# Performance work log

Measured on AMD Instinct MI355X. Metric: run time of the kernel, lower is better.

The kernel has to match this reference:

```python
import jax, jax.numpy as jnp
from jax import lax
import numpy as np

DEPTH, D_MODEL, D_INNER, D_STATE, DT_RANK = 24, 192, 384, 16, 12
EPS = 1e-5

def _layernorm(x, w, b):
    m = x.mean(-1, keepdims=True)
    v = ((x - m) ** 2).mean(-1, keepdims=True)
    return (x - m) * lax.rsqrt(v + EPS) * w + b

def _silu(x):
    return x * jax.nn.sigmoid(x)

def _mamba_mixer(x, in_w, cw, cb, xp_w, dtw, dtb, a_log, dvec, out_w):
    # x: (B, L, D_MODEL)
    B, L, _ = x.shape
    xz = jnp.einsum('bld,ed->ble', x, in_w)            # (B, L, 2*D_INNER)
    xi, z = xz[..., :D_INNER], xz[..., D_INNER:]
    # causal depthwise conv1d, kernel 4 (left-pad 3, truncate to L)
    xt = jnp.moveaxis(xi, 1, 2)                        # (B, D_INNER, L)
    xt = jnp.pad(xt, ((0, 0), (0, 0), (3, 0)))
    xt = lax.conv_general_dilated(xt, cw[:, None, :], (1,), 'VALID',
                                  dimension_numbers=('NCH', 'OIH', 'NCH'),
                                  feature_group_count=D_INNER)
    xt = _silu(xt + cb[None, :, None])
    xc = jnp.moveaxis(xt, 1, 2)                        # (B, L, D_INNER)
    x_dbl = jnp.einsum('bld,ed->ble', xc, xp_w)        # (B, L, DT_RANK+2*D_STATE)
    dt = x_dbl[..., :DT_RANK]
    Bm = x_dbl[..., DT_RANK:DT_RANK + D_STATE]         # (B, L, N)
    Cm = x_dbl[..., DT_RANK + D_STATE:]                # (B, L, N)
    delta = jax.nn.softplus(jnp.einsum('blr,dr->bld', dt, dtw) + dtb)  # (B, L, D_INNER)
    A = -jnp.exp(a_log)                                # (D_INNER, N)
    dA = jnp.exp(delta[..., None] * A)                 # (B, L, D_INNER, N)
    dBx = (delta * xc)[..., None] * Bm[:, :, None, :]  # (B, L, D_INNER, N)

    def step(h, inp):
        dA_t, dBx_t, C_t = inp
        h = dA_t * h + dBx_t
        y = jnp.einsum('bdn,bn->bd', h, C_t)
        return h, y

    h0 = jnp.zeros((B, D_INNER, D_STATE), x.dtype)
    _, ys = lax.scan(step, h0, (jnp.moveaxis(dA, 1, 0), jnp.moveaxis(dBx, 1, 0), jnp.moveaxis(Cm, 1, 0)))
    y = jnp.moveaxis(ys, 0, 1) + xc * dvec             # (B, L, D_INNER)
    y = y * _silu(z)
    return jnp.einsum('ble,de->bld', y, out_w)

def _forward(x, patch_w, patch_b, norm_w, norm_b, in_proj_w, conv_w, conv_b,
             x_proj_w, dt_w, dt_b, A_log, Dp, out_proj_w, normf_w, normf_b, head_w, head_b):
    # patch embed: conv 16x16 stride 16 -> (B, 192, 14, 14) -> (B, 196, 192)
    h = lax.conv_general_dilated(x, patch_w, (16, 16), 'VALID',
                                 dimension_numbers=('NCHW', 'OIHW', 'NCHW'))
    h = h + patch_b[None, :, None, None]
    B = h.shape[0]
    hidden = h.reshape(B, D_MODEL, -1).transpose(0, 2, 1)  # (B, L, D)
    residual = None
    for d in range(DEPTH):
        residual = hidden if residual is None else residual + hidden
        normed = _layernorm(residual, norm_w[d], norm_b[d])
        hidden = _mamba_mixer(normed, in_proj_w[d], conv_w[d], conv_b[d], x_proj_w[d],
                              dt_w[d], dt_b[d], A_log[d], Dp[d], out_proj_w[d])
    residual = residual + hidden
    feat = _layernorm(residual, normf_w, normf_b)
    pooled = feat.mean(axis=1)                           # final_pool_type='mean'
    return pooled @ head_w.T + head_b                    # (B, num_classes)

def setup_inputs() -> dict:
    key = jax.random.key(0)
    ks = jax.random.split(key, 16)
    s = 0.05
    return {
        'x': jax.random.normal(ks[0], (64, 3, 224, 224), jnp.float32),
        'patch_w': jax.random.normal(ks[1], (192, 3, 16, 16), jnp.float32) * s,
        'patch_b': jnp.zeros((192,), jnp.float32),
        'norm_w': jnp.ones((DEPTH, D_MODEL), jnp.float32),
        'norm_b': jnp.zeros((DEPTH, D_MODEL), jnp.float32),
        'in_proj_w': jax.random.normal(ks[2], (DEPTH, 2 * D_INNER, D_MODEL), jnp.float32) * s,
        'conv_w': jax.random.normal(ks[3], (DEPTH, D_INNER, 4), jnp.float32) * 0.3,
        'conv_b': jnp.zeros((DEPTH, D_INNER), jnp.float32),
        'x_proj_w': jax.random.normal(ks[4], (DEPTH, DT_RANK + 2 * D_STATE, D_INNER), jnp.float32) * s,
        'dt_w': jax.random.normal(ks[5], (DEPTH, D_INNER, DT_RANK), jnp.float32) * s,
        'dt_b': jax.random.uniform(ks[6], (DEPTH, D_INNER), jnp.float32, -4.0, -2.0),
        'A_log': jnp.log(jnp.broadcast_to(jnp.arange(1, D_STATE + 1, dtype=jnp.float32), (DEPTH, D_INNER, D_STATE))),
        'Dp': jnp.ones((DEPTH, D_INNER), jnp.float32),
        'out_proj_w': jax.random.normal(ks[7], (DEPTH, D_MODEL, D_INNER), jnp.float32) * s,
        'normf_w': jnp.ones((D_MODEL,), jnp.float32),
        'normf_b': jnp.zeros((D_MODEL,), jnp.float32),
        'head_w': jax.random.normal(ks[8], (1000, D_MODEL), jnp.float32) * s,
        'head_b': jnp.zeros((1000,), jnp.float32),
    }

def reference(x, patch_w, patch_b, norm_w, norm_b, in_proj_w, conv_w, conv_b,
              x_proj_w, dt_w, dt_b, A_log, Dp, out_proj_w, normf_w, normf_b, head_w, head_b):
    return _forward(x, patch_w, patch_b, norm_w, norm_b, in_proj_w, conv_w, conv_b,
                    x_proj_w, dt_w, dt_b, A_log, Dp, out_proj_w, normf_w, normf_b, head_w, head_b)
```

## Files before the change

### kernel.cpp

```cpp
#include <hip/hip_runtime.h>
#include <math.h>


#define DEPTH 24
#define DM 192
#define DI 384
#define DS 16
#define DR 12
#define SEQL 196
#define BATCH 64
#define MROWS (BATCH*SEQL)
#define XDP 8624
#define LOG2E 1.44269504088896340736f

typedef unsigned short ushort_t;
typedef __bf16 bf16x8 __attribute__((ext_vector_type(8)));
typedef float f32x4 __attribute__((ext_vector_type(4)));

__device__ __forceinline__ float sigmoidf_(float x) { return 1.f / (1.f + __expf(-x)); }

__device__ __forceinline__ ushort_t f2bf(float f) {
    union { float f; unsigned u; } c; c.f = f;
    unsigned u = c.u;
    return (ushort_t)((u + 0x7FFFu + ((u >> 16) & 1u)) >> 16);
}
__device__ __forceinline__ float bf2f(ushort_t u) {
    union { unsigned u; float f; } c; c.u = ((unsigned)u) << 16;
    return c.f;
}

__device__ __forceinline__ void load_lds16(const ushort_t* g, ushort_t* l) {
    __builtin_amdgcn_global_load_lds((__attribute__((address_space(1))) void*)g,
                                     (__attribute__((address_space(3))) void*)l, 16, 0, 0);
}

template<int CTRL>
__device__ __forceinline__ float dpp_mov(float oldv, float src) {
    return __builtin_bit_cast(float, __builtin_amdgcn_update_dpp(
        __builtin_bit_cast(int, oldv), __builtin_bit_cast(int, src),
        CTRL, 0xF, 0xF, false));
}

template<int CTRL, bool LAST>
__device__ __forceinline__ void ks_step(float* P, float* h) {
    #pragma unroll
    for (int n = 0; n < DS; n++) {
        float Hp = dpp_mov<CTRL>(0.f, h[n]);
        float Pp = LAST ? 1.f : dpp_mov<CTRL>(1.f, P[n]);
        h[n] = fmaf(P[n], Hp, h[n]);
        if (!LAST) P[n] *= Pp;
    }
}

__global__ void f2bf4_kernel(const float* __restrict__ src, ushort_t* __restrict__ dst, int n4) {
    int i = blockIdx.x * 256 + threadIdx.x;
    if (i >= n4) return;
    float4 v = ((const float4*)src)[i];
    union { ushort_t s[4]; uint2 u; } o;
    o.s[0] = f2bf(v.x); o.s[1] = f2bf(v.y); o.s[2] = f2bf(v.z); o.s[3] = f2bf(v.w);
    ((uint2*)dst)[i] = o.u;
}

__global__ void xp_pad_kernel(const float* __restrict__ src, ushort_t* __restrict__ dst) {
    int i = blockIdx.x * 256 + threadIdx.x;
    if (i >= DEPTH * 64 * 384) return;
    int col = i % 384, row = (i / 384) & 63, d = i / (384 * 64);
    float v = (row < 44) ? src[(size_t)d * 44 * 384 + row * 384 + col] : 0.f;
    dst[i] = f2bf(v);
}

template<bool BF>
__global__ void ln_kernel(float* __restrict__ residual, const float* __restrict__ hidden,
                          const float* __restrict__ w, const float* __restrict__ b,
                          void* __restrict__ out_) {
    int wave = threadIdx.x >> 6, lane = threadIdx.x & 63;
    int row = blockIdx.x * 4 + wave;
    float* rr = residual + (size_t)row * DM;
    const float* hr = hidden + (size_t)row * DM;
    float v0 = rr[lane]       + hr[lane];
    float v1 = rr[lane + 64]  + hr[lane + 64];
    float v2 = rr[lane + 128] + hr[lane + 128];
    rr[lane] = v0; rr[lane + 64] = v1; rr[lane + 128] = v2;
    float s = v0 + v1 + v2;
    #pragma unroll
    for (int off = 32; off > 0; off >>= 1) s += __shfl_down(s, off);
    float mean = __shfl(s, 0) * (1.f / DM);
    float d0 = v0 - mean, d1 = v1 - mean, d2 = v2 - mean;
    float q = d0 * d0 + d1 * d1 + d2 * d2;
    #pragma unroll
    for (int off = 32; off > 0; off >>= 1) q += __shfl_down(q, off);
    float rstd = rsqrtf(__shfl(q, 0) * (1.f / DM) + 1e-5f);
    float o0 = d0 * rstd * w[lane]       + b[lane];
    float o1 = d1 * rstd * w[lane + 64]  + b[lane + 64];
    float o2 = d2 * rstd * w[lane + 128] + b[lane + 128];
    if constexpr (BF) {
        ushort_t* o = (ushort_t*)out_ + (size_t)row * DM;
        o[lane] = f2bf(o0); o[lane + 64] = f2bf(o1); o[lane + 128] = f2bf(o2);
    } else {
        float* o = (float*)out_ + (size_t)row * DM;
        o[lane] = o0; o[lane + 64] = o1; o[lane + 128] = o2;
    }
}

template<int BN, int WM, int WN, int NST, bool TC>
__global__ __launch_bounds__(256, 2) void gemm_mfma(const ushort_t* __restrict__ A,
        const ushort_t* __restrict__ W, float* __restrict__ C, int K, int ldC) {
    constexpr int FM = 128 / (WM * 16);
    constexpr int FN = BN / (WN * 16);
    __shared__ ushort_t sA[128 * 32];
    __shared__ ushort_t sB[BN * 32];
    const int t = threadIdx.x;
    const int wave = t >> 6, lane = t & 63;
    const int lr = lane & 15, lq = lane >> 4;
    const int wr = wave / WN, wc = wave % WN;
    const int m0 = blockIdx.x * 128, n0 = blockIdx.y * BN;
    const int wbase = t & ~63;

    f32x4 acc[FM][FN];
    #pragma unroll
    for (int i = 0; i < FM; i++)
        #pragma unroll
        for (int j = 0; j < FN; j++) acc[i][j] = f32x4{0.f, 0.f, 0.f, 0.f};

    for (int k0 = 0; k0 < K; k0 += 32) {
        __syncthreads();
        #pragma unroll
        for (int c = 0; c < 2; c++) {
            int s = c * 256 + t;
            int row = s >> 2;
            int quad = (s & 3) ^ ((row >> 1) & 3);
            load_lds16(A + (size_t)(m0 + row) * K + k0 + quad * 8,
                       sA + (size_t)(c * 256 + wbase) * 8);
        }
        #pragma unroll
        for (int c = 0; c < BN * 4 / 256; c++) {
            int s = c * 256 + t;
            int row = s >> 2;
            int quad = (s & 3) ^ ((row >> 1) & 3);
            load_lds16(W + (size_t)(n0 + row) * K + k0 + quad * 8,
                       sB + (size_t)(c * 256 + wbase) * 8);
        }
        __syncthreads();
        bf16x8 af[FM], bfr[FN];
        #pragma unroll
        for (int i = 0; i < FM; i++) {
            int row = wr * FM * 16 + i * 16 + lr;
            int slot = (row << 2) | (lq ^ ((row >> 1) & 3));
            af[i] = *(const bf16x8*)&sA[(size_t)slot * 8];
        }
        #pragma unroll
        for (int j = 0; j < FN; j++) {
            int row = wc * FN * 16 + j * 16 + lr;
            int slot = (row << 2) | (lq ^ ((row >> 1) & 3));
            bfr[j] = *(const bf16x8*)&sB[(size_t)slot * 8];
        }
        #pragma unroll
        for (int i = 0; i < FM; i++)
            #pragma unroll
            for (int j = 0; j < FN; j++)
                acc[i][j] = __builtin_amdgcn_mfma_f32_16x16x32_bf16(af[i], bfr[j], acc[i][j], 0, 0, 0);
    }
    int crow0 = m0 + wr * FM * 16 + lq * 4;
    int ccol0 = n0 + wc * FN * 16 + lr;
    if constexpr (TC) {
        #pragma unroll
        for (int i = 0; i < FM; i++) {
            int m = crow0 + i * 16;
            int bb = m / 196, l = m % 196;
            #pragma unroll
            for (int j = 0; j < FN; j++) {
                int col = ccol0 + j * 16;
                if (col < 44) {
                    float4 v = {acc[i][j][0], acc[i][j][1], acc[i][j][2], acc[i][j][3]};
                    *(float4*)(C + (size_t)bb * XDP + (size_t)col * 196 + l) = v;
                }
            }
        }
    } else {
        #pragma unroll
        for (int i = 0; i < FM; i++)
            #pragma unroll
            for (int j = 0; j < FN; j++) {
                if (wc * FN + j >= NST) continue;
                float* cp = C + (size_t)(crow0 + i * 16) * ldC + ccol0 + j * 16;
                #pragma unroll
                for (int r = 0; r < 4; r++) cp[(size_t)r * ldC] = acc[i][j][r];
            }
    }
}

__global__ __launch_bounds__(256, 2) void gemm_patch_mfma(const ushort_t* __restrict__ Xbf,
        const ushort_t* __restrict__ Wbf, const float* __restrict__ bias, float* __restrict__ C) {
    constexpr int FM = 2, FN = 4;
    __shared__ ushort_t sA[128 * 32];
    __shared__ ushort_t sB[64 * 32];
    const int t = threadIdx.x;
    const int wave = t >> 6, lane = t & 63;
    const int lr = lane & 15, lq = lane >> 4;
    const int m0 = blockIdx.x * 128, n0 = blockIdx.y * 64;
    const int wbase = t & ~63;

    const ushort_t* abase[2];
    int aquad[2];
    #pragma unroll
    for (int c = 0; c < 2; c++) {
        int s = c * 256 + t;
        int row = s >> 2;
        aquad[c] = (s & 3) ^ ((row >> 1) & 3);
        int m = m0 + row;
        int b = m / 196, r = m % 196, py = r / 14, px = r % 14;
        abase[c] = Xbf + (size_t)b * 150528 + py * 3584 + px * 16;
    }
    int brow = t >> 2;
    int bquad = (t & 3) ^ ((brow >> 1) & 3);
    const ushort_t* bbase = Wbf + (size_t)(n0 + brow) * 768 + bquad * 8;

    f32x4 acc[FM][FN];
    #pragma unroll
    for (int i = 0; i < FM; i++)
        #pragma unroll
        for (int j = 0; j < FN; j++) acc[i][j] = f32x4{0.f, 0.f, 0.f, 0.f};

    for (int k0 = 0; k0 < 768; k0 += 32) {
        __syncthreads();
        #pragma unroll
        for (int c = 0; c < 2; c++) {
            int k = k0 + aquad[c] * 8;
            int ci = k >> 8, ky = (k >> 4) & 15, kx0 = k & 15;
            load_lds16(abase[c] + ci * 50176 + ky * 224 + kx0,
                       sA + (size_t)(c * 256 + wbase) * 8);
        }
        load_lds16(bbase + k0, sB + (size_t)wbase * 8);
        __syncthreads();
        bf16x8 af[FM], bfr[FN];
        #pragma unroll
        for (int i = 0; i < FM; i++) {
            int row = wave * FM * 16 + i * 16 + lr;
            int slot = (row << 2) | (lq ^ ((row >> 1) & 3));
            af[i] = *(const bf16x8*)&sA[(size_t)slot * 8];
        }
        #pragma unroll
        for (int j = 0; j < FN; j++) {
            int row = j * 16 + lr;
            int slot = (row << 2) | (lq ^ ((row >> 1) & 3));
            bfr[j] = *(const bf16x8*)&sB[(size_t)slot * 8];
        }
        #pragma unroll
        for (int i = 0; i < FM; i++)
            #pragma unroll
            for (int j = 0; j < FN; j++)
                acc[i][j] = __builtin_amdgcn_mfma_f32_16x16x32_bf16(af[i], bfr[j], acc[i][j], 0, 0, 0);
    }
    int crow0 = m0 + wave * FM * 16 + lq * 4;
    int ccol0 = n0 + lr;
    #pragma unroll
    for (int i = 0; i < FM; i++)
        #pragma unroll
        for (int j = 0; j < FN; j++) {
            int col = ccol0 + j * 16;
            float bv = bias[col];
            float* cp = C + (size_t)(crow0 + i * 16) * DM + col;
            #pragma unroll
            for (int r = 0; r < 4; r++) cp[(size_t)r * DM] = acc[i][j][r] + bv;
        }
}

template<bool BIAS>
__global__ __launch_bounds__(256, 2) void gemm64(const float* __restrict__ A,
        const float* __restrict__ W, const float* __restrict__ bias,
        float* __restrict__ C, int M, int N, int K) {
    __shared__ float As[32][68];
    __shared__ float Ws[32][68];
    int t = threadIdx.x;
    int m0 = blockIdx.x * 64, n0 = blockIdx.y * 64;
    int lr = t >> 2, lk = (t & 3) * 4;
    int am = m0 + lr; bool avld = am < M;
    const float* Ap = A + (size_t)(avld ? am : 0) * K + lk;
    int wn = n0 + lr; bool wv = wn < N;
    const float* Wp = W + (size_t)(wv ? wn : 0) * K + lk;
    int tm = (t >> 4) * 4, tn = (t & 15) * 4;
    float acc[4][4];
    #pragma unroll
    for (int i = 0; i < 4; i++)
        #pragma unroll
        for (int j = 0; j < 4; j++) acc[i][j] = 0.f;

    for (int k0 = 0; k0 < K; k0 += 32) {
        float4 a0 = make_float4(0.f, 0.f, 0.f, 0.f), a1 = a0, w0 = a0, w1 = a0;
        if (avld) { a0 = *(const float4*)(Ap + k0); a1 = *(const float4*)(Ap + k0 + 16); }
        if (wv)   { w0 = *(const float4*)(Wp + k0); w1 = *(const float4*)(Wp + k0 + 16); }
        __syncthreads();
        As[lk + 0][lr] = a0.x; As[lk + 1][lr] = a0.y; As[lk + 2][lr] = a0.z; As[lk + 3][lr] = a0.w;
        As[lk + 16][lr] = a1.x; As[lk + 17][lr] = a1.y; As[lk + 18][lr] = a1.z; As[lk + 19][lr] = a1.w;
        Ws[lk + 0][lr] = w0.x; Ws[lk + 1][lr] = w0.y; Ws[lk + 2][lr] = w0.z; Ws[lk + 3][lr] = w0.w;
        Ws[lk + 16][lr] = w1.x; Ws[lk + 17][lr] = w1.y; Ws[lk + 18][lr] = w1.z; Ws[lk + 19][lr] = w1.w;
        __syncthreads();
        #pragma unroll
        for (int kk = 0; kk < 32; kk++) {
            float4 x0 = *(const float4*)&As[kk][tm];
            float4 y0 = *(const float4*)&Ws[kk][tn];
            float av[4] = {x0.x, x0.y, x0.z, x0.w};
            float bv[4] = {y0.x, y0.y, y0.z, y0.w};
            #pragma unroll
            for (int i = 0; i < 4; i++)
                #pragma unroll
                for (int j = 0; j < 4; j++) acc[i][j] = fmaf(av[i], bv[j], acc[i][j]);
        }
    }
    #pragma unroll
    for (int i = 0; i < 4; i++) {
        int m = m0 + tm + i;
        if (m >= M) continue;
        float* cr = C + (size_t)m * N;
        int n = n0 + tn;
        if (n < N) {
            float4 v = {acc[i][0], acc[i][1], acc[i][2], acc[i][3]};
            if (BIAS) { v.x += bias[n]; v.y += bias[n + 1]; v.z += bias[n + 2]; v.w += bias[n + 3]; }
            *(float4*)(cr + n) = v;
        }
    }
}

__global__ void conv_silu_kernel(const float* __restrict__ xz, const float* __restrict__ cw,
                                 const float* __restrict__ cb, ushort_t* __restrict__ xcbf) {
    int idx = blockIdx.x * 256 + threadIdx.x;
    if (idx >= MROWS * DI) return;
    int e = idx % DI; int bl = idx / DI; int l = bl % SEQL; int b = bl / SEQL;
    const float* base = xz + (size_t)(b * SEQL) * 768 + e;
    float w0 = cw[e * 4], w1 = cw[e * 4 + 1], w2 = cw[e * 4 + 2], w3 = cw[e * 4 + 3];
    float acc = cb[e];
    if (l >= 3) acc = fmaf(base[(size_t)(l - 3) * 768], w0, acc);
    if (l >= 2) acc = fmaf(base[(size_t)(l - 2) * 768], w1, acc);
    if (l >= 1) acc = fmaf(base[(size_t)(l - 1) * 768], w2, acc);
    acc = fmaf(base[(size_t)l * 768], w3, acc);
    xcbf[idx] = f2bf(acc * sigmoidf_(acc));
}

__global__ __launch_bounds__(512, 4) void scan_kernel(const float* __restrict__ xdt,
        const ushort_t* __restrict__ xcbf, const float* __restrict__ xz,
        const float* __restrict__ dtw, const float* __restrict__ dtb,
        const float* __restrict__ a_log, const float* __restrict__ Dp, ushort_t* __restrict__ y) {
    __shared__ float sd[44 * 196];
    __shared__ ushort_t zs[8 * 200];
    __shared__ ushort_t xcs[8 * 200];
    __shared__ ushort_t ys[8 * 200];
    __shared__ float avs[8][16];
    __shared__ float wdts[8][16];
    const int b = blockIdx.x, eg = blockIdx.y;
    const int tid = threadIdx.x;
    const int wave = tid >> 6, lane = tid & 63;
    const int e = eg * 8 + wave;

    {
        const float4* src4 = (const float4*)(xdt + (size_t)b * XDP);
        float4* sd4 = (float4*)sd;
        for (int i = tid; i < XDP / 4; i += 512) sd4[i] = src4[i];
    }
    if (lane < DS) avs[wave][lane] = -__expf(a_log[(size_t)e * DS + lane]) * LOG2E;
    if (lane >= 16 && lane < 16 + DR) wdts[wave][lane - 16] = dtw[(size_t)e * DR + (lane - 16)];
    if (tid < 196) {
        int l = tid;
        const ushort_t* xp = xcbf + (size_t)(b * SEQL + l) * DI + eg * 8;
        ushort4 xq0 = *(const ushort4*)xp;
        ushort4 xq1 = *(const ushort4*)(xp + 4);
        const float* zp = xz + (size_t)(b * SEQL + l) * 768 + DI + eg * 8;
        float4 zq0 = *(const float4*)zp;
        float4 zq1 = *(const float4*)(zp + 4);
        xcs[0 * 200 + l] = xq0.x; xcs[1 * 200 + l] = xq0.y;
        xcs[2 * 200 + l] = xq0.z; xcs[3 * 200 + l] = xq0.w;
        xcs[4 * 200 + l] = xq1.x; xcs[5 * 200 + l] = xq1.y;
        xcs[6 * 200 + l] = xq1.z; xcs[7 * 200 + l] = xq1.w;
        zs[0 * 200 + l] = f2bf(zq0.x); zs[1 * 200 + l] = f2bf(zq0.y);
        zs[2 * 200 + l] = f2bf(zq0.z); zs[3 * 200 + l] = f2bf(zq0.w);
        zs[4 * 200 + l] = f2bf(zq1.x); zs[5 * 200 + l] = f2bf(zq1.y);
        zs[6 * 200 + l] = f2bf(zq1.z); zs[7 * 200 + l] = f2bf(zq1.w);
    }
    __syncthreads();

    const float db = dtb[e];
    const bool act = lane < 49;
    const int lbase = act ? lane * 4 : 0;

    f32x4 dt4 = {db, db, db, db};
    #pragma unroll
    for (int k = 0; k < DR; k++) {
        f32x4 r = *(const f32x4*)&sd[k * 196 + lbase];
        dt4 += r * wdts[wave][k];
    }
    f32x4 d4;
    #pragma unroll
    for (int s = 0; s < 4; s++) {
        float v = dt4[s];
        d4[s] = (v > 20.f) ? v : __logf(1.f + __expf(v));
    }
    f32x4 du4;
    {
        ushort4 xcq = *(const ushort4*)&xcs[wave * 200 + lbase];
        du4 = d4 * f32x4{bf2f(xcq.x), bf2f(xcq.y), bf2f(xcq.z), bf2f(xcq.w)};
    }

    float P[DS], h[DS];
    #pragma unroll
    for (int n = 0; n < DS; n++) { P[n] = 1.f; h[n] = 0.f; }
    if (act) {
        #pragma unroll
        for (int n = 0; n < DS; n++) {
            float Avn = avs[wave][n];
            f32x4 Bn = *(const f32x4*)&sd[(12 + n) * 196 + lbase];
            float hn = 0.f, Pn = 1.f;
            #pragma unroll
            for (int s = 0; s < 4; s++) {
                float dA = __builtin_amdgcn_exp2f(d4[s] * Avn);
                hn = fmaf(hn, dA, du4[s] * Bn[s]);
                Pn *= dA;
            }
            P[n] = Pn; h[n] = hn;
        }
    }

    ks_step<0x111, false>(P, h);
    ks_step<0x112, false>(P, h);
    ks_step<0x114, false>(P, h);
    ks_step<0x118, false>(P, h);
    ks_step<0x142, false>(P, h);
    ks_step<0x143, true >(P, h);

    #pragma unroll
    for (int n = 0; n < DS; n++) {
        float Hp = __shfl_up(h[n], 1);
        h[n] = (lane == 0) ? 0.f : Hp;
    }

    if (act) {
        f32x4 acc4 = {0.f, 0.f, 0.f, 0.f};
        #pragma unroll
        for (int n = 0; n < DS; n++) {
            float Avn = avs[wave][n];
            f32x4 Bn = *(const f32x4*)&sd[(12 + n) * 196 + lbase];
            f32x4 Cn = *(const f32x4*)&sd[(28 + n) * 196 + lbase];
            float hn = h[n];
            #pragma unroll
            for (int s = 0; s < 4; s++) {
                float dA = __builtin_amdgcn_exp2f(d4[s] * Avn);
                hn = fmaf(hn, dA, du4[s] * Bn[s]);
                acc4[s] = fmaf(hn, Cn[s], acc4[s]);
            }
        }
        ushort4 xcq = *(const ushort4*)&xcs[wave * 200 + lbase];
        f32x4 xcv4 = {bf2f(xcq.x), bf2f(xcq.y), bf2f(xcq.z), bf2f(xcq.w)};
        ushort4 zq = *(const ushort4*)&zs[wave * 200 + lbase];
        f32x4 zv4 = {bf2f(zq.x), bf2f(zq.y), bf2f(zq.z), bf2f(zq.w)};
        const float Dv = Dp[e];
        ushort_t* yw = &ys[wave * 200 + lbase];
        #pragma unroll
        for (int s = 0; s < 4; s++) {
            float yv = fmaf(xcv4[s], Dv, acc4[s]);
            float zv = zv4[s];
            yw[s] = f2bf(yv * zv * sigmoidf_(zv));
        }
    }
    __syncthreads();
    if (tid < 196) {
        int l = tid;
        ushort4 o0, o1;
        o0.x = ys[0 * 200 + l]; o0.y = ys[1 * 200 + l];
        o0.z = ys[2 * 200 + l]; o0.w = ys[3 * 200 + l];
        o1.x = ys[4 * 200 + l]; o1.y = ys[5 * 200 + l];
        o1.z = ys[6 * 200 + l]; o1.w = ys[7 * 200 + l];
        ushort_t* yp = y + (size_t)(b * SEQL + l) * DI + eg * 8;
        *(ushort4*)yp = o0;
        *(ushort4*)(yp + 4) = o1;
    }
}

__global__ void pool_kernel(const float* __restrict__ normed, float* __restrict__ pooled) {
    int b = blockIdx.x, d = threadIdx.x;
    float s = 0.f;
    for (int l = 0; l < SEQL; l++) s += normed[(size_t)(b * SEQL + l) * DM + d];
    pooled[b * DM + d] = s * (1.f / 196.f);
}

extern "C" void kernel_launch(void* const* d_in, const int* in_sizes, int n_in,
                              void* d_out, int out_size, void* d_ws, size_t ws_size,
                              hipStream_t stream) {
    const float* x       = (const float*)d_in[0];
    const float* patch_w = (const float*)d_in[1];
    const float* patch_b = (const float*)d_in[2];
    const float* norm_w  = (const float*)d_in[3];
    const float* norm_b  = (const float*)d_in[4];
    const float* in_w    = (const float*)d_in[5];
    const float* conv_w  = (const float*)d_in[6];
    const float* conv_b  = (const float*)d_in[7];
    const float* xp_w    = (const float*)d_in[8];
    const float* dt_w    = (const float*)d_in[9];
    const float* dt_b    = (const float*)d_in[10];
    const float* A_log   = (const float*)d_in[11];
    const float* Dp      = (const float*)d_in[12];
    const float* out_w   = (const float*)d_in[13];
    const float* normf_w = (const float*)d_in[14];
    const float* normf_b = (const float*)d_in[15];
    const float* head_w  = (const float*)d_in[16];
    const float* head_b  = (const float*)d_in[17];

    float* ws = (float*)d_ws;
    float* residual     = ws;
    float* hidden       = ws + 2408448;
    float* xz           = ws + 4816896;
    ushort_t* xcbf      = (ushort_t*)(ws + 14450688);
    ushort_t* y_bf      = (ushort_t*)(ws + 16859136);
    ushort_t* x_bf      = (ushort_t*)(ws + 14450688);
    ushort_t* normed_bf = (ushort_t*)(ws + 19267584);
    float* xdbl_t       = ws + 20471808;
    float* pooled       = ws + 21023744;
    ushort_t* in_w_bf   = (ushort_t*)(ws + 21036032);
    ushort_t* out_w_bf  = (ushort_t*)(ws + 22805504);
    ushort_t* xp_w_bf   = (ushort_t*)(ws + 23690240);
    ushort_t* patch_w_bf= (ushort_t*)(ws + 23985152);

    (void)hipMemsetAsync(residual, 0, (size_t)2408448 * sizeof(float), stream);

    f2bf4_kernel<<<3456, 256, 0, stream>>>(in_w, in_w_bf, 884736);
    f2bf4_kernel<<<1728, 256, 0, stream>>>(out_w, out_w_bf, 442368);
    f2bf4_kernel<<<144, 256, 0, stream>>>(patch_w, patch_w_bf, 36864);
    f2bf4_kernel<<<9408, 256, 0, stream>>>(x, x_bf, 2408448);
    xp_pad_kernel<<<2304, 256, 0, stream>>>(xp_w, xp_w_bf);

    gemm_patch_mfma<<<dim3(98, 3), 256, 0, stream>>>(x_bf, patch_w_bf, patch_b, hidden);

    for (int d = 0; d < DEPTH; ++d) {
        ln_kernel<true><<<3136, 256, 0, stream>>>(residual, hidden, norm_w + d * DM,
                                                  norm_b + d * DM, normed_bf);
        gemm_mfma<192, 2, 2, 12, false><<<dim3(98, 4), 256, 0, stream>>>(normed_bf,
                in_w_bf + (size_t)d * 768 * 192, xz, 192, 768);
        conv_silu_kernel<<<18816, 256, 0, stream>>>(xz, conv_w + d * DI * 4, conv_b + d * DI, xcbf);
        gemm_mfma<64, 4, 1, 3, true><<<dim3(98, 1), 256, 0, stream>>>(xcbf,
                xp_w_bf + (size_t)d * 64 * 384, xdbl_t, 384, 196);
        scan_kernel<<<dim3(64, 48), 512, 0, stream>>>(xdbl_t, xcbf, xz, dt_w + d * DI * DR,
                dt_b + d * DI, A_log + d * DI * DS, Dp + d * DI, y_bf);
        gemm_mfma<64, 4, 1, 4, false><<<dim3(98, 3), 256, 0, stream>>>(y_bf,
                out_w_bf + (size_t)d * 192 * 384, hidden, 384, 192);
    }

    ln_kernel<false><<<3136, 256, 0, stream>>>(residual, hidden, normf_w, normf_b, xz);
    pool_kernel<<<64, 192, 0, stream>>>(xz, pooled);
    gemm64<true><<<dim3(1, 16), 256, 0, stream>>>(pooled, head_w, head_b, (float*)d_out, 64, 1000, 192);
}
```

Measured before the change: 3.167 ms.

## Remap selective scan lanes to state-by-time-chunk with DPP state reduction

```diff
diff --git a/kernel.cpp b/kernel.cpp
--- a/kernel.cpp
+++ b/kernel.cpp
@@ -41,15 +41,12 @@
         CTRL, 0xF, 0xF, false));
 }
 
-template<int CTRL, bool LAST>
-__device__ __forceinline__ void ks_step(float* P, float* h) {
-    #pragma unroll
-    for (int n = 0; n < DS; n++) {
-        float Hp = dpp_mov<CTRL>(0.f, h[n]);
-        float Pp = LAST ? 1.f : dpp_mov<CTRL>(1.f, P[n]);
-        h[n] = fmaf(P[n], Hp, h[n]);
-        if (!LAST) P[n] *= Pp;
-    }
+__device__ __forceinline__ float row16_sum(float v) {
+    v += dpp_mov<0xB1>(0.f, v);
+    v += dpp_mov<0x4E>(0.f, v);
+    v += dpp_mov<0x141>(0.f, v);
+    v += dpp_mov<0x140>(0.f, v);
+    return v;
 }
 
 __global__ void f2bf4_kernel(const float* __restrict__ src, ushort_t* __restrict__ dst, int n4) {
@@ -336,27 +333,27 @@
     xcbf[idx] = f2bf(acc * sigmoidf_(acc));
 }
 
-__global__ __launch_bounds__(512, 4) void scan_kernel(const float* __restrict__ xdt,
+__global__ __launch_bounds__(512, 6) void scan_kernel(const float* __restrict__ xdt,
         const ushort_t* __restrict__ xcbf, const float* __restrict__ xz,
         const float* __restrict__ dtw, const float* __restrict__ dtb,
         const float* __restrict__ a_log, const float* __restrict__ Dp, ushort_t* __restrict__ y) {
     __shared__ float sd[44 * 196];
+    __shared__ float dls[8][196];
     __shared__ ushort_t zs[8 * 200];
     __shared__ ushort_t xcs[8 * 200];
     __shared__ ushort_t ys[8 * 200];
-    __shared__ float avs[8][16];
     __shared__ float wdts[8][16];
     const int b = blockIdx.x, eg = blockIdx.y;
     const int tid = threadIdx.x;
     const int wave = tid >> 6, lane = tid & 63;
     const int e = eg * 8 + wave;
+    const int n = lane & 15, c = lane >> 4;
 
     {
         const float4* src4 = (const float4*)(xdt + (size_t)b * XDP);
         float4* sd4 = (float4*)sd;
         for (int i = tid; i < XDP / 4; i += 512) sd4[i] = src4[i];
     }
-    if (lane < DS) avs[wave][lane] = -__expf(a_log[(size_t)e * DS + lane]) * LOG2E;
     if (lane >= 16 && lane < 16 + DR) wdts[wave][lane - 16] = dtw[(size_t)e * DR + (lane - 16)];
     if (tid < 196) {
         int l = tid;
@@ -377,86 +374,85 @@
     }
     __syncthreads();
 
+    const float Avn = -__expf(a_log[(size_t)e * DS + n]) * LOG2E;
     const float db = dtb[e];
-    const bool act = lane < 49;
-    const int lbase = act ? lane * 4 : 0;
-
-    f32x4 dt4 = {db, db, db, db};
-    #pragma unroll
-    for (int k = 0; k < DR; k++) {
-        f32x4 r = *(const f32x4*)&sd[k * 196 + lbase];
-        dt4 += r * wdts[wave][k];
-    }
-    f32x4 d4;
-    #pragma unroll
-    for (int s = 0; s < 4; s++) {
-        float v = dt4[s];
-        d4[s] = (v > 20.f) ? v : __logf(1.f + __expf(v));
-    }
-    f32x4 du4;
+
+    if (lane < 49) {
+        const int lb = lane * 4;
+        f32x4 dt4 = {db, db, db, db};
+        #pragma unroll
+        for (int k = 0; k < DR; k++) {
+            f32x4 r = *(const f32x4*)&sd[k * 196 + lb];
+            dt4 += r * wdts[wave][k];
+        }
+        f32x4 d4;
+        #pragma unroll
+        for (int s = 0; s < 4; s++) {
+            float v = dt4[s];
+            d4[s] = (v > 20.f) ? v : __logf(1.f + __expf(v));
+        }
+        *(f32x4*)&dls[wave][lb] = d4;
+    }
+
+    const int t0 = (c == 0) ? 0 : 48 * c + 4;
+    const int iters = (c == 0) ? 13 : 12;
+    const float* Brow = &sd[(12 + n) * 196];
+    const float* Crow = &sd[(28 + n) * 196];
+    const float* dlw = dls[wave];
+    const ushort_t* xcw = &xcs[wave * 200];
+
+    float h = 0.f;
+    f32x4 dsum = {0.f, 0.f, 0.f, 0.f};
+    for (int i = 0; i < iters; i++) {
+        int t = t0 + 4 * i;
+        f32x4 dl = *(const f32x4*)&dlw[t];
+        f32x4 Bn = *(const f32x4*)&Brow[t];
+        ushort4 xcq = *(const ushort4*)&xcw[t];
+        const ushort_t* xcp = (const ushort_t*)&xcq;
+        dsum += dl;
+        #pragma unroll
+        for (int s = 0; s < 4; s++) {
+            float dA = __builtin_amdgcn_exp2f(dl[s] * Avn);
+            h = fmaf(h, dA, (dl[s] * bf2f(xcp[s])) * Bn[s]);
+        }
+    }
+    float P = __builtin_amdgcn_exp2f(Avn * (dsum[0] + dsum[1] + dsum[2] + dsum[3]));
+
     {
-        ushort4 xcq = *(const ushort4*)&xcs[wave * 200 + lbase];
-        du4 = d4 * f32x4{bf2f(xcq.x), bf2f(xcq.y), bf2f(xcq.z), bf2f(xcq.w)};
-    }
-
-    float P[DS], h[DS];
-    #pragma unroll
-    for (int n = 0; n < DS; n++) { P[n] = 1.f; h[n] = 0.f; }
-    if (act) {
-        #pragma unroll
-        for (int n = 0; n < DS; n++) {
-            float Avn = avs[wave][n];
-            f32x4 Bn = *(const f32x4*)&sd[(12 + n) * 196 + lbase];
-            float hn = 0.f, Pn = 1.f;
-            #pragma unroll
-            for (int s = 0; s < 4; s++) {
-                float dA = __builtin_amdgcn_exp2f(d4[s] * Avn);
-                hn = fmaf(hn, dA, du4[s] * Bn[s]);
-                Pn *= dA;
-            }
-            P[n] = Pn; h[n] = hn;
-        }
-    }
-
-    ks_step<0x111, false>(P, h);
-    ks_step<0x112, false>(P, h);
-    ks_step<0x114, false>(P, h);
-    ks_step<0x118, false>(P, h);
-    ks_step<0x142, false>(P, h);
-    ks_step<0x143, true >(P, h);
-
-    #pragma unroll
-    for (int n = 0; n < DS; n++) {
-        float Hp = __shfl_up(h[n], 1);
-        h[n] = (lane == 0) ? 0.f : Hp;
-    }
-
-    if (act) {
-        f32x4 acc4 = {0.f, 0.f, 0.f, 0.f};
-        #pragma unroll
-        for (int n = 0; n < DS; n++) {
-            float Avn = avs[wave][n];
-            f32x4 Bn = *(const f32x4*)&sd[(12 + n) * 196 + lbase];
-            f32x4 Cn = *(const f32x4*)&sd[(28 + n) * 196 + lbase];
-            float hn = h[n];
-            #pragma unroll
-            for (int s = 0; s < 4; s++) {
-                float dA = __builtin_amdgcn_exp2f(d4[s] * Avn);
-                hn = fmaf(hn, dA, du4[s] * Bn[s]);
-                acc4[s] = fmaf(hn, Cn[s], acc4[s]);
-            }
-        }
-        ushort4 xcq = *(const ushort4*)&xcs[wave * 200 + lbase];
-        f32x4 xcv4 = {bf2f(xcq.x), bf2f(xcq.y), bf2f(xcq.z), bf2f(xcq.w)};
-        ushort4 zq = *(const ushort4*)&zs[wave * 200 + lbase];
-        f32x4 zv4 = {bf2f(zq.x), bf2f(zq.y), bf2f(zq.z), bf2f(zq.w)};
-        const float Dv = Dp[e];
-        ushort_t* yw = &ys[wave * 200 + lbase];
+        float hp = __shfl_up(h, 16), pp = __shfl_up(P, 16);
+        if (c >= 1) { h = fmaf(P, hp, h); P *= pp; }
+        hp = __shfl_up(h, 32); pp = __shfl_up(P, 32);
+        if (c >= 2) { h = fmaf(P, hp, h); P *= pp; }
+    }
+    float hin = __shfl_up(h, 16);
+    if (c == 0) hin = 0.f;
+
+    const float Dv = Dp[e];
+    const ushort_t* zw = &zs[wave * 200];
+    ushort_t* yw = &ys[wave * 200];
+    h = hin;
+    for (int i = 0; i < iters; i++) {
+        int t = t0 + 4 * i;
+        f32x4 dl = *(const f32x4*)&dlw[t];
+        f32x4 Bn = *(const f32x4*)&Brow[t];
+        f32x4 Cn = *(const f32x4*)&Crow[t];
+        ushort4 xcq = *(const ushort4*)&xcw[t];
+        const ushort_t* xcp = (const ushort_t*)&xcq;
+        f32x4 yp;
         #pragma unroll
         for (int s = 0; s < 4; s++) {
-            float yv = fmaf(xcv4[s], Dv, acc4[s]);
-            float zv = zv4[s];
-            yw[s] = f2bf(yv * zv * sigmoidf_(zv));
+            float dA = __builtin_amdgcn_exp2f(dl[s] * Avn);
+            h = fmaf(h, dA, (dl[s] * bf2f(xcp[s])) * Bn[s]);
+            yp[s] = h * Cn[s];
+        }
+        #pragma unroll
+        for (int s = 0; s < 4; s++) yp[s] = row16_sum(yp[s]);
+        if (n < 4) {
+            float ysel = (n == 0) ? yp[0] : (n == 1) ? yp[1] : (n == 2) ? yp[2] : yp[3];
+            float xcsel = bf2f((n == 0) ? xcp[0] : (n == 1) ? xcp[1] : (n == 2) ? xcp[2] : xcp[3]);
+            float zv = bf2f(zw[t + n]);
+            float yv = fmaf(xcsel, Dv, ysel);
+            yw[t + n] = f2bf(yv * zv * sigmoidf_(zv));
         }
     }
     __syncthreads();
```

After: 3.365 ms. 1.06x slower.
